# Performance work log

Hardware: AMD Instinct MI355X
Metric: run time of the kernel (lower is better)

The kernel has to match this reference:

```python
import jax, jax.numpy as jnp
import numpy as np

B, T, D, H = 4, 2048, 1024, 16
HS = D // H  # head_size = 64
EPS = 1e-5


def _layernorm(x, g, b):
    mu = jnp.mean(x, axis=-1, keepdims=True)
    var = jnp.var(x, axis=-1, keepdims=True)
    return (x - mu) * jax.lax.rsqrt(var + EPS) * g + b


def setup_inputs() -> dict:
    key = jax.random.key(0)
    ks = jax.random.split(key, 12)
    s = lambda fan_in: 1.0 / np.sqrt(fan_in)
    return {
        "x": jax.random.normal(ks[0], (B, T, D), dtype=jnp.float32),
        # per-head projections, stacked: (H, D, HS)
        "Wq": jax.random.uniform(ks[1], (H, D, HS), jnp.float32, -s(D), s(D)),
        "Wk": jax.random.uniform(ks[2], (H, D, HS), jnp.float32, -s(D), s(D)),
        "Wv": jax.random.uniform(ks[3], (H, D, HS), jnp.float32, -s(D), s(D)),
        "Wo": jax.random.uniform(ks[4], (D, D), jnp.float32, -s(D), s(D)),
        "bo": jax.random.uniform(ks[5], (D,), jnp.float32, -s(D), s(D)),
        "W1": jax.random.uniform(ks[6], (D, 4 * D), jnp.float32, -s(D), s(D)),
        "b1": jax.random.uniform(ks[7], (4 * D,), jnp.float32, -s(D), s(D)),
        "W2": jax.random.uniform(ks[8], (4 * D, D), jnp.float32, -s(4 * D), s(4 * D)),
        "b2": jax.random.uniform(ks[9], (D,), jnp.float32, -s(4 * D), s(4 * D)),
        "g1": jnp.ones((D,), jnp.float32),
        "be1": jnp.zeros((D,), jnp.float32),
        "g2": jnp.ones((D,), jnp.float32),
        "be2": jnp.zeros((D,), jnp.float32),
    }


def reference(x, Wq, Wk, Wv, Wo, bo, W1, b1, W2, b2, g1, be1, g2, be2):
    # --- self-attention sublayer (pre-LN) ---
    h = _layernorm(x, g1, be1)                       # (B,T,D)
    q = jnp.einsum('btd,hds->bhts', h, Wq)           # (B,H,T,HS)
    k = jnp.einsum('btd,hds->bhts', h, Wk)
    v = jnp.einsum('btd,hds->bhts', h, Wv)
    scores = jnp.einsum('bhts,bhus->bhtu', q, k) * (HS ** -0.5)  # (B,H,T,T)
    causal = jnp.tril(jnp.ones((T, T), dtype=bool))
    scores = jnp.where(causal, scores, -jnp.inf)
    w = jax.nn.softmax(scores, axis=-1)
    attn = jnp.einsum('bhtu,bhus->bhts', w, v)       # (B,H,T,HS)
    attn = attn.transpose(0, 2, 1, 3).reshape(B, T, D)  # concat heads
    x = x + attn @ Wo + bo
    # --- feed-forward sublayer (pre-LN) ---
    h2 = _layernorm(x, g2, be2)
    x = x + jax.nn.relu(h2 @ W1 + b1) @ W2 + b2
    return x
```

## Files before the change

### kernel.cpp

```cpp
#include <hip/hip_runtime.h>
#include <hip/hip_bf16.h>
#include <cstddef>

#define B_ 4
#define T_ 2048
#define D_ 1024
#define H_ 16
#define HS_ 64
#define QS_ 3072

typedef short short8 __attribute__((ext_vector_type(8)));
typedef float f32x4 __attribute__((ext_vector_type(4)));

__device__ __forceinline__ unsigned short f2b(float x) {
    __hip_bfloat16 b = __float2bfloat16(x);
    return *reinterpret_cast<unsigned short*>(&b);
}

__device__ __forceinline__ void gload_lds16(const void* g, void* l) {
    __builtin_amdgcn_global_load_lds((const __attribute__((address_space(1))) void*)g,
                                     (__attribute__((address_space(3))) void*)l, 16, 0, 0);
}

__global__ __launch_bounds__(256) void ln_kernel(const float* __restrict__ X,
                                                 const float* __restrict__ g,
                                                 const float* __restrict__ be,
                                                 unsigned short* __restrict__ O)
{
    const int row = blockIdx.x;
    const int tid = threadIdx.x;
    const float* xr = X + (size_t)row * D_;
    float4 xv = *reinterpret_cast<const float4*>(xr + tid * 4);
    float s  = xv.x + xv.y + xv.z + xv.w;
    float s2 = xv.x * xv.x + xv.y * xv.y + xv.z * xv.z + xv.w * xv.w;
#pragma unroll
    for (int off = 32; off > 0; off >>= 1) {
        s  += __shfl_xor(s,  off);
        s2 += __shfl_xor(s2, off);
    }
    __shared__ float red[8];
    const int wid = tid >> 6, lane = tid & 63;
    if (lane == 0) { red[wid * 2] = s; red[wid * 2 + 1] = s2; }
    __syncthreads();
    s  = red[0] + red[2] + red[4] + red[6];
    s2 = red[1] + red[3] + red[5] + red[7];
    const float mu  = s * (1.0f / D_);
    const float var = s2 * (1.0f / D_) - mu * mu;
    const float r   = rsqrtf(var + 1e-5f);
    float4 gv = *reinterpret_cast<const float4*>(g  + tid * 4);
    float4 bv = *reinterpret_cast<const float4*>(be + tid * 4);
    ushort4 ov;
    ov.x = f2b((xv.x - mu) * r * gv.x + bv.x);
    ov.y = f2b((xv.y - mu) * r * gv.y + bv.y);
    ov.z = f2b((xv.z - mu) * r * gv.z + bv.z);
    ov.w = f2b((xv.w - mu) * r * gv.w + bv.w);
    *reinterpret_cast<ushort4*>(O + (size_t)row * D_ + tid * 4) = ov;
}

__global__ __launch_bounds__(256) void transpose_all(const float* __restrict__ Wq,
                                                     const float* __restrict__ Wk,
                                                     const float* __restrict__ Wv,
                                                     const float* __restrict__ Wo,
                                                     const float* __restrict__ W1,
                                                     const float* __restrict__ W2,
                                                     unsigned short* __restrict__ Wtqkv,
                                                     unsigned short* __restrict__ Wto,
                                                     unsigned short* __restrict__ Wt1,
                                                     unsigned short* __restrict__ Wt2)
{
    __shared__ float tile[32][33];
    const int tx = threadIdx.x & 31, ty = threadIdx.x >> 5;
    int s = blockIdx.x;

    if (s < 3072) {
        const float* in = (s < 1024) ? Wq : (s < 2048) ? Wk : Wv;
        const int noff = (s < 1024) ? 0 : (s < 2048) ? D_ : 2 * D_;
        s &= 1023;
        const int bn = (s & 31) * 32, bk = (s >> 5) * 32;
        const int head = bn >> 6, s0 = bn & 63;
#pragma unroll
        for (int i = 0; i < 32; i += 8)
            tile[ty + i][tx] = in[(size_t)head * D_ * HS_ + (size_t)(bk + ty + i) * HS_ + s0 + tx];
        __syncthreads();
#pragma unroll
        for (int i = 0; i < 32; i += 8)
            Wtqkv[(size_t)(noff + bn + ty + i) * D_ + bk + tx] = f2b(tile[tx][ty + i]);
        return;
    }
    s -= 3072;
    const float* in; unsigned short* out; int K, N, bn, bk;
    if (s < 1024)      { in = Wo; out = Wto; K = D_;     N = D_;     bn = (s & 31) * 32;  bk = (s >> 5) * 32; }
    else if (s < 5120) { s -= 1024; in = W1; out = Wt1; K = D_;     N = 4 * D_; bn = (s & 127) * 32; bk = (s >> 7) * 32; }
    else               { s -= 5120; in = W2; out = Wt2; K = 4 * D_; N = D_;     bn = (s & 31) * 32;  bk = (s >> 5) * 32; }
#pragma unroll
    for (int i = 0; i < 32; i += 8)
        tile[ty + i][tx] = in[(size_t)(bk + ty + i) * N + bn + tx];
    __syncthreads();
#pragma unroll
    for (int i = 0; i < 32; i += 8)
        out[(size_t)(bn + ty + i) * K + bk + tx] = f2b(tile[tx][ty + i]);
}

template<bool BIAS, bool RELU, bool RESID, bool OUT_BF16, bool SCALEQ>
__global__ __launch_bounds__(512, 1) void gemm_sq(const unsigned short* __restrict__ A,
                                                  const unsigned short* __restrict__ Bt,
                                                  const float* __restrict__ bias,
                                                  const float* __restrict__ resid,
                                                  float* __restrict__ Cf,
                                                  unsigned short* __restrict__ Cb,
                                                  int M, int N, int K)
{
    constexpr int BUFS = 16384 + 16384;
    __shared__ __attribute__((aligned(128))) unsigned short lds[2 * BUFS];

    const int tid = threadIdx.x, l = tid & 63, w = tid >> 6;
    const int wRow = w >> 2, wCol = w & 3;
    const int lr = l & 15, lq = l >> 4;

    const int gx = gridDim.x;
    const int nwg = gx * (int)gridDim.y;
    const int orig = (int)blockIdx.y * gx + (int)blockIdx.x;
    const int xcd = orig & 7, lo = orig >> 3;
    const int q8 = nwg >> 3, r8 = nwg & 7;
    const int wg = (xcd < r8 ? xcd * (q8 + 1) : r8 * (q8 + 1) + (xcd - r8) * q8) + lo;
    const int bm = wg / gx, bn = wg % gx;

    const int nt = K >> 6;

    auto ISSUE_HALF = [&](int t, int half) {
        const size_t kof = (size_t)t * 64;
        const int buf = t & 1;
        const unsigned short* src = (half < 2) ? A : Bt;
        const int rb = ((half < 2) ? bm : bn) * 256 + (half & 1) * 128;
        const int lb = buf * BUFS + ((half >= 2) ? 16384 : 0) + (half & 1) * 128 * 64;
#pragma unroll
        for (int p = 0; p < 2; ++p) {
            const int j = p * 512 + tid;
            const int row = j >> 3, ci = j & 7;
            gload_lds16(src + (size_t)(rb + row) * K + kof + ((ci ^ (row & 7)) * 8),
                        &lds[lb + j * 8]);
        }
    };

    f32x4 acc[8][4];
#pragma unroll
    for (int i = 0; i < 8; ++i)
#pragma unroll
        for (int j = 0; j < 4; ++j) acc[i][j] = (f32x4){0.f, 0.f, 0.f, 0.f};

    short8 af[4][2], bf[4][2];
    const int swz = lr & 7;

#pragma unroll
    for (int h = 0; h < 4; ++h) ISSUE_HALF(0, h);

    for (int t = 0; t < nt; ++t) {
        const unsigned short* As = &lds[(t & 1) * BUFS];
        const unsigned short* Bs = As + 16384;
        const bool more = (t + 1 < nt);

        asm volatile("s_waitcnt vmcnt(0)" ::: "memory");
        __builtin_amdgcn_s_barrier();

        if (more) ISSUE_HALF(t + 1, 0);
#pragma unroll
        for (int mi = 0; mi < 4; ++mi) {
            const int row = wRow * 128 + mi * 16 + lr;
#pragma unroll
            for (int ks = 0; ks < 2; ++ks)
                af[mi][ks] = *reinterpret_cast<const short8*>(&As[row * 64 + (((ks * 4 + lq) ^ swz) * 8)]);
        }
#pragma unroll
        for (int nj = 0; nj < 2; ++nj) {
            const int rowB = wCol * 64 + nj * 16 + lr;
#pragma unroll
            for (int ks = 0; ks < 2; ++ks)
                bf[nj][ks] = *reinterpret_cast<const short8*>(&Bs[rowB * 64 + (((ks * 4 + lq) ^ swz) * 8)]);
        }
        asm volatile("s_waitcnt lgkmcnt(0)" ::: "memory");
        __builtin_amdgcn_sched_barrier(0);
        __builtin_amdgcn_s_setprio(1);
#pragma unroll
        for (int mi = 0; mi < 4; ++mi)
#pragma unroll
            for (int nj = 0; nj < 2; ++nj)
#pragma unroll
                for (int ks = 0; ks < 2; ++ks)
                    acc[mi][nj] = __builtin_amdgcn_mfma_f32_16x16x32_bf16(af[mi][ks], bf[nj][ks], acc[mi][nj], 0, 0, 0);
        __builtin_amdgcn_s_setprio(0);

        if (more) ISSUE_HALF(t + 1, 1);
#pragma unroll
        for (int nj = 2; nj < 4; ++nj) {
            const int rowB = wCol * 64 + nj * 16 + lr;
#pragma unroll
            for (int ks = 0; ks < 2; ++ks)
                bf[nj][ks] = *reinterpret_cast<const short8*>(&Bs[rowB * 64 + (((ks * 4 + lq) ^ swz) * 8)]);
        }
        asm volatile("s_waitcnt lgkmcnt(0)" ::: "memory");
        __builtin_amdgcn_sched_barrier(0);
        __builtin_amdgcn_s_setprio(1);
#pragma unroll
        for (int mi = 0; mi < 4; ++mi)
#pragma unroll
            for (int nj = 2; nj < 4; ++nj)
#pragma unroll
                for (int ks = 0; ks < 2; ++ks)
                    acc[mi][nj] = __builtin_amdgcn_mfma_f32_16x16x32_bf16(af[mi][ks], bf[nj][ks], acc[mi][nj], 0, 0, 0);
        __builtin_amdgcn_s_setprio(0);

        if (more) { ISSUE_HALF(t + 1, 2); ISSUE_HALF(t + 1, 3); }
#pragma unroll
        for (int mi = 0; mi < 4; ++mi) {
            const int row = wRow * 128 + (4 + mi) * 16 + lr;
#pragma unroll
            for (int ks = 0; ks < 2; ++ks)
                af[mi][ks] = *reinterpret_cast<const short8*>(&As[row * 64 + (((ks * 4 + lq) ^ swz) * 8)]);
        }
        asm volatile("s_waitcnt lgkmcnt(0)" ::: "memory");
        __builtin_amdgcn_sched_barrier(0);
        __builtin_amdgcn_s_setprio(1);
#pragma unroll
        for (int mi = 0; mi < 4; ++mi)
#pragma unroll
            for (int nj = 0; nj < 2; ++nj)
#pragma unroll
                for (int ks = 0; ks < 2; ++ks)
                    acc[4 + mi][nj] = __builtin_amdgcn_mfma_f32_16x16x32_bf16(af[mi][ks], bf[nj][ks], acc[4 + mi][nj], 0, 0, 0);
        __builtin_amdgcn_s_setprio(0);

        __builtin_amdgcn_s_setprio(1);
#pragma unroll
        for (int mi = 0; mi < 4; ++mi)
#pragma unroll
            for (int nj = 2; nj < 4; ++nj)
#pragma unroll
                for (int ks = 0; ks < 2; ++ks)
                    acc[4 + mi][nj] = __builtin_amdgcn_mfma_f32_16x16x32_bf16(af[mi][ks], bf[nj][ks], acc[4 + mi][nj], 0, 0, 0);
        __builtin_amdgcn_s_setprio(0);
    }

    const int m0 = bm * 256 + wRow * 128;
    const int n0 = bn * 256 + wCol * 64;
#pragma unroll
    for (int nf = 0; nf < 4; ++nf) {
        const int col = n0 + nf * 16 + lr;
        const float bv = BIAS ? bias[col] : 0.0f;
#pragma unroll
        for (int mf = 0; mf < 8; ++mf) {
#pragma unroll
            for (int r = 0; r < 4; ++r) {
                const int row = m0 + mf * 16 + lq * 4 + r;
                float c = acc[mf][nf][r] + bv;
                if (RELU) c = fmaxf(c, 0.0f);
                if (RESID) c += resid[(size_t)row * N + col];
                if (SCALEQ) { if (col < D_) c *= 0.18033688f; }
                if (OUT_BF16) Cb[(size_t)row * N + col] = f2b(c);
                else          Cf[(size_t)row * N + col] = c;
            }
        }
    }
}

template<bool BIAS, bool RELU, bool RESID, bool OUT_BF16, bool SCALEQ>
__global__ __launch_bounds__(512, 1) void gemm_sq2(const unsigned short* __restrict__ A,
                                                   const unsigned short* __restrict__ Bt,
                                                   const float* __restrict__ bias,
                                                   const float* __restrict__ resid,
                                                   float* __restrict__ Cf,
                                                   unsigned short* __restrict__ Cb,
                                                   int M, int N, int K)
{
    constexpr int BUFS = 8192 + 16384;
    __shared__ __attribute__((aligned(128))) unsigned short lds[3 * BUFS];

    const int tid = threadIdx.x, l = tid & 63, w = tid >> 6;
    const int wRow = w >> 2, wCol = w & 3;
    const int lr = l & 15, lq = l >> 4;

    const int gx = gridDim.x;
    const int nwg = gx * (int)gridDim.y;
    const int orig = (int)blockIdx.y * gx + (int)blockIdx.x;
    const int xcd = orig & 7, lo = orig >> 3;
    const int q8 = nwg >> 3, r8 = nwg & 7;
    const int wg = (xcd < r8 ? xcd * (q8 + 1) : r8 * (q8 + 1) + (xcd - r8) * q8) + lo;
    const int bm = wg / gx, bn = wg % gx;

    const int nt = K >> 6;

    auto ISSUE = [&](int t, int buf) {
        const size_t kof = (size_t)t * 64;
#pragma unroll
        for (int p = 0; p < 2; ++p) {
            const int j = p * 512 + tid;
            const int row = j >> 3, ci = j & 7;
            gload_lds16(A + (size_t)(bm * 128 + row) * K + kof + ((ci ^ (row & 7)) * 8),
                        &lds[buf * BUFS + j * 8]);
        }
#pragma unroll
        for (int p = 0; p < 4; ++p) {
            const int j = p * 512 + tid;
            const int row = j >> 3, ci = j & 7;
            gload_lds16(Bt + (size_t)(bn * 256 + row) * K + kof + ((ci ^ (row & 7)) * 8),
                        &lds[buf * BUFS + 8192 + j * 8]);
        }
    };

    f32x4 acc[4][4];
#pragma unroll
    for (int i = 0; i < 4; ++i)
#pragma unroll
        for (int j = 0; j < 4; ++j) acc[i][j] = (f32x4){0.f, 0.f, 0.f, 0.f};

    short8 af[2][2], bf[4][2];
    const int swz = lr & 7;

    ISSUE(0, 0);
    ISSUE(1, 1);

    for (int t = 0; t < nt; ++t) {
        const unsigned short* As = &lds[(t % 3) * BUFS];
        const unsigned short* Bs = As + 8192;
        if (t + 1 < nt) asm volatile("s_waitcnt vmcnt(6)" ::: "memory");
        else            asm volatile("s_waitcnt vmcnt(0)" ::: "memory");
        __builtin_amdgcn_s_barrier();
        if (t + 2 < nt) ISSUE(t + 2, (t + 2) % 3);

#pragma unroll
        for (int mi = 0; mi < 2; ++mi) {
            const int row = wRow * 64 + mi * 16 + lr;
#pragma unroll
            for (int ks = 0; ks < 2; ++ks)
                af[mi][ks] = *reinterpret_cast<const short8*>(&As[row * 64 + (((ks * 4 + lq) ^ swz) * 8)]);
        }
#pragma unroll
        for (int nj = 0; nj < 4; ++nj) {
            const int rowB = wCol * 64 + nj * 16 + lr;
#pragma unroll
            for (int ks = 0; ks < 2; ++ks)
                bf[nj][ks] = *reinterpret_cast<const short8*>(&Bs[rowB * 64 + (((ks * 4 + lq) ^ swz) * 8)]);
        }
        asm volatile("s_waitcnt lgkmcnt(0)" ::: "memory");
        __builtin_amdgcn_sched_barrier(0);
        __builtin_amdgcn_s_setprio(1);
#pragma unroll
        for (int mi = 0; mi < 2; ++mi)
#pragma unroll
            for (int nj = 0; nj < 4; ++nj)
#pragma unroll
                for (int ks = 0; ks < 2; ++ks)
                    acc[mi][nj] = __builtin_amdgcn_mfma_f32_16x16x32_bf16(af[mi][ks], bf[nj][ks], acc[mi][nj], 0, 0, 0);
        __builtin_amdgcn_s_setprio(0);

#pragma unroll
        for (int mi = 0; mi < 2; ++mi) {
            const int row = wRow * 64 + (2 + mi) * 16 + lr;
#pragma unroll
            for (int ks = 0; ks < 2; ++ks)
                af[mi][ks] = *reinterpret_cast<const short8*>(&As[row * 64 + (((ks * 4 + lq) ^ swz) * 8)]);
        }
        asm volatile("s_waitcnt lgkmcnt(0)" ::: "memory");
        __builtin_amdgcn_sched_barrier(0);
        __builtin_amdgcn_s_setprio(1);
#pragma unroll
        for (int mi = 0; mi < 2; ++mi)
#pragma unroll
            for (int nj = 0; nj < 4; ++nj)
#pragma unroll
                for (int ks = 0; ks < 2; ++ks)
                    acc[2 + mi][nj] = __builtin_amdgcn_mfma_f32_16x16x32_bf16(af[mi][ks], bf[nj][ks], acc[2 + mi][nj], 0, 0, 0);
        __builtin_amdgcn_s_setprio(0);
    }

    const int m0 = bm * 128 + wRow * 64;
    const int n0 = bn * 256 + wCol * 64;
#pragma unroll
    for (int nf = 0; nf < 4; ++nf) {
        const int col = n0 + nf * 16 + lr;
        const float bv = BIAS ? bias[col] : 0.0f;
#pragma unroll
        for (int mf = 0; mf < 4; ++mf) {
#pragma unroll
            for (int r = 0; r < 4; ++r) {
                const int row = m0 + mf * 16 + lq * 4 + r;
                float c = acc[mf][nf][r] + bv;
                if (RELU) c = fmaxf(c, 0.0f);
                if (RESID) c += resid[(size_t)row * N + col];
                if (SCALEQ) { if (col < D_) c *= 0.18033688f; }
                if (OUT_BF16) Cb[(size_t)row * N + col] = f2b(c);
                else          Cf[(size_t)row * N + col] = c;
            }
        }
    }
}

template<bool MASKED>
__device__ __forceinline__ void attn_chunk(
    const unsigned short* __restrict__ ksb,
    const unsigned short (* __restrict__ vsb)[72],
    unsigned short (* __restrict__ psw)[72],
    const short8* aq, f32x4* o,
    int lr, int lq, int wl)
{
    const short8 vone = {0x3F80, 0x3F80, 0x3F80, 0x3F80, 0x3F80, 0x3F80, 0x3F80, 0x3F80};
    f32x4 s[4];
#pragma unroll
    for (int kb = 0; kb < 4; ++kb) s[kb] = (f32x4){0.f, 0.f, 0.f, 0.f};
    __builtin_amdgcn_s_setprio(1);
#pragma unroll
    for (int kb = 0; kb < 4; ++kb) {
        if (MASKED && kb > wl) continue;
        const int row = kb * 16 + lr;
        const int sw = row & 7;
#pragma unroll
        for (int ks = 0; ks < 2; ++ks) {
            const int ch = (ks * 4 + lq) ^ sw;
            const short8 bk = *reinterpret_cast<const short8*>(&ksb[row * 64 + ch * 8]);
            s[kb] = __builtin_amdgcn_mfma_f32_16x16x32_bf16(aq[ks], bk, s[kb], 0, 0, 0);
        }
    }
    __builtin_amdgcn_s_setprio(0);

#pragma unroll
    for (int r = 0; r < 4; ++r) {
        const int qloc = wl * 16 + lq * 4 + r;
        float p[4];
#pragma unroll
        for (int kb = 0; kb < 4; ++kb) {
            const bool msk = MASKED && (kb * 16 + lr > qloc);
            p[kb] = msk ? 0.0f : exp2f(s[kb][r]);
        }
        const unsigned int w0 = (unsigned int)f2b(p[0]) | ((unsigned int)f2b(p[1]) << 16);
        const unsigned int w1 = (unsigned int)f2b(p[2]) | ((unsigned int)f2b(p[3]) << 16);
        uint2 pk; pk.x = w0; pk.y = w1;
        *reinterpret_cast<uint2*>(&psw[lq * 4 + r][lr * 4]) = pk;
    }
    asm volatile("s_waitcnt lgkmcnt(0)" ::: "memory");
    __builtin_amdgcn_s_setprio(1);
#pragma unroll
    for (int ks = 0; ks < 2; ++ks) {
        const short8 pa = *reinterpret_cast<const short8*>(&psw[lr][ks * 32 + lq * 8]);
#pragma unroll
        for (int df = 0; df < 4; ++df) {
            const short8 vb = *reinterpret_cast<const short8*>(&vsb[df * 16 + lr][ks * 32 + lq * 8]);
            o[df] = __builtin_amdgcn_mfma_f32_16x16x32_bf16(pa, vb, o[df], 0, 0, 0);
        }
        o[4] = __builtin_amdgcn_mfma_f32_16x16x32_bf16(pa, vone, o[4], 0, 0, 0);
    }
    __builtin_amdgcn_s_setprio(0);
}

__global__ __launch_bounds__(512, 4) void attn_mfma(const unsigned short* __restrict__ QKV,
                                                    unsigned short* __restrict__ Og)
{
    __shared__ __attribute__((aligned(128))) unsigned short Ks[2][64 * 64];
    __shared__ __attribute__((aligned(16)))  unsigned short Vs[2][64][72];
    __shared__ __attribute__((aligned(16)))  unsigned short Ps[8][16][72];

    const int NQT = T_ / 128;
    const int px = blockIdx.x;
    const int qtA = px, qtB = NQT - 1 - px;
    const int h = blockIdx.y, b = blockIdx.z;
    const int tid = threadIdx.x, w = tid >> 6, l = tid & 63;
    const int wl = w & 3, qsub = w >> 2;
    const int lr = l & 15, lq = l >> 4;
    const size_t base = (size_t)b * T_ * QS_ + h * HS_;

    short8 aqA[2], aqB[2];
    {
        const int qrl = qsub * 64 + wl * 16 + lr;
        const unsigned short* pA = QKV + base + (size_t)(qtA * 128 + qrl) * QS_;
        const unsigned short* pB = QKV + base + (size_t)(qtB * 128 + qrl) * QS_;
        aqA[0] = *reinterpret_cast<const short8*>(pA + lq * 8);
        aqA[1] = *reinterpret_cast<const short8*>(pA + 32 + lq * 8);
        aqB[0] = *reinterpret_cast<const short8*>(pB + lq * 8);
        aqB[1] = *reinterpret_cast<const short8*>(pB + 32 + lq * 8);
    }

    const unsigned short* Kg = QKV + D_;
    const unsigned short* Vg = QKV + 2 * D_;

    auto stage = [&](int c, int bf) {
        const int kbase = c * 64;
        {
            const int row = tid >> 3;
            const int c8 = ((tid & 7) ^ (row & 7)) * 8;
            gload_lds16(Kg + base + (size_t)(kbase + row) * QS_ + c8,
                        &Ks[bf][tid * 8]);
        }
        {
            const int vkey = tid & 63, vd0 = (tid >> 6) * 8;
            const int jkey = (vkey & 15) * 4 + (vkey >> 4);
            const unsigned short* vsrc = Vg + base + (size_t)(kbase + vkey) * QS_ + vd0;
            short8 v0 = *reinterpret_cast<const short8*>(vsrc);
#pragma unroll
            for (int jj = 0; jj < 8; ++jj) Vs[bf][vd0 + jj][jkey] = (unsigned short)v0[jj];
        }
    };

    stage(0, 0);
    __syncthreads();

    unsigned short (*psw)[72] = Ps[w];

    f32x4 oA[5], oB[5];
#pragma unroll
    for (int df = 0; df < 5; ++df) {
        oA[df] = (f32x4){0.f, 0.f, 0.f, 0.f};
        oB[df] = (f32x4){0.f, 0.f, 0.f, 0.f};
    }

    const int qminw = qsub * 64 + wl * 16;
    const int qmaxw = qminw + 15;

    const int nch = 2 * qtB + 2;
    int bf = 0;
    for (int c = 0; c < nch; ++c) {
        if (c + 1 < nch) stage(c + 1, bf ^ 1);
        const int relA = c * 64 - qtA * 128;
        const int relB = c * 64 - qtB * 128;
        if (relA <= qmaxw) {
            if (relA + 63 <= qminw)
                attn_chunk<false>(&Ks[bf][0], Vs[bf], psw, aqA, oA, lr, lq, wl);
            else
                attn_chunk<true>(&Ks[bf][0], Vs[bf], psw, aqA, oA, lr, lq, wl);
        }
        if (relB <= qmaxw) {
            if (relB + 63 <= qminw)
                attn_chunk<false>(&Ks[bf][0], Vs[bf], psw, aqB, oB, lr, lq, wl);
            else
                attn_chunk<true>(&Ks[bf][0], Vs[bf], psw, aqB, oB, lr, lq, wl);
        }
        if (c + 1 < nch) __syncthreads();
        bf ^= 1;
    }

    const size_t obase = (size_t)b * T_ * D_ + h * HS_;
#pragma unroll
    for (int r = 0; r < 4; ++r) {
        const float invA = 1.0f / oA[4][r];
        const float invB = 1.0f / oB[4][r];
        const int qrl = qsub * 64 + wl * 16 + lq * 4 + r;
        unsigned short* orowA = Og + obase + (size_t)(qtA * 128 + qrl) * D_;
        unsigned short* orowB = Og + obase + (size_t)(qtB * 128 + qrl) * D_;
#pragma unroll
        for (int df = 0; df < 4; ++df) {
            orowA[df * 16 + lr] = f2b(oA[df][r] * invA);
            orowB[df * 16 + lr] = f2b(oB[df][r] * invB);
        }
    }
}

extern "C" void kernel_launch(void* const* d_in, const int* in_sizes, int n_in,
                              void* d_out, int out_size, void* d_ws, size_t ws_size,
                              hipStream_t stream)
{
    const float* x   = (const float*)d_in[0];
    const float* Wq  = (const float*)d_in[1];
    const float* Wk  = (const float*)d_in[2];
    const float* Wv  = (const float*)d_in[3];
    const float* Wo  = (const float*)d_in[4];
    const float* bo  = (const float*)d_in[5];
    const float* W1  = (const float*)d_in[6];
    const float* b1  = (const float*)d_in[7];
    const float* W2  = (const float*)d_in[8];
    const float* b2  = (const float*)d_in[9];
    const float* g1  = (const float*)d_in[10];
    const float* be1 = (const float*)d_in[11];
    const float* g2  = (const float*)d_in[12];
    const float* be2 = (const float*)d_in[13];
    float* out = (float*)d_out;

    unsigned short* ws = (unsigned short*)d_ws;
    const size_t NT = (size_t)B_ * T_;
    unsigned short* hb    = ws;
    unsigned short* QKVb  = hb + NT * D_;
    unsigned short* Ab    = QKVb + NT * 3 * D_;
    unsigned short* f1    = QKVb;
    unsigned short* Wtqkv = Ab + NT * D_;
    unsigned short* Wto   = Wtqkv + (size_t)3 * D_ * D_;
    unsigned short* Wt1   = Wto + (size_t)D_ * D_;
    unsigned short* Wt2   = Wt1 + (size_t)4 * D_ * D_;

    dim3 b256(256), b512(512);

    transpose_all<<<dim3(12288), b256, 0, stream>>>(Wq, Wk, Wv, Wo, W1, W2,
                                                    Wtqkv, Wto, Wt1, Wt2);

    ln_kernel<<<NT, b256, 0, stream>>>(x, g1, be1, hb);

    gemm_sq2<false, false, false, true, true><<<dim3(3 * D_ / 256, NT / 128), b512, 0, stream>>>(
        hb, Wtqkv, nullptr, nullptr, nullptr, QKVb, (int)NT, 3 * D_, D_);

    attn_mfma<<<dim3(T_ / 256, H_, B_), b512, 0, stream>>>(QKVb, Ab);

    gemm_sq2<true, false, true, false, false><<<dim3(D_ / 256, NT / 128), b512, 0, stream>>>(
        Ab, Wto, bo, x, out, nullptr, (int)NT, D_, D_);

    ln_kernel<<<NT, b256, 0, stream>>>(out, g2, be2, hb);

    gemm_sq<true, true, false, true, false><<<dim3(4 * D_ / 256, NT / 256), b512, 0, stream>>>(
        hb, Wt1, b1, nullptr, nullptr, f1, (int)NT, 4 * D_, D_);

    gemm_sq2<true, false, true, false, false><<<dim3(D_ / 256, NT / 128), b512, 0, stream>>>(
        f1, Wt2, b2, out, out, nullptr, (int)NT, D_, 4 * D_);
}
```

Baseline: 342.7 us.

## Write V transposed from QKV GEMM epilogue and stage it via direct LDS loads

```diff
diff --git a/kernel.cpp b/kernel.cpp
--- a/kernel.cpp
+++ b/kernel.cpp
@@ -262,13 +262,14 @@
     }
 }
 
-template<bool BIAS, bool RELU, bool RESID, bool OUT_BF16, bool SCALEQ>
+template<bool BIAS, bool RELU, bool RESID, bool OUT_BF16, bool SCALEQ, bool VSPLIT>
 __global__ __launch_bounds__(512, 1) void gemm_sq2(const unsigned short* __restrict__ A,
                                                    const unsigned short* __restrict__ Bt,
                                                    const float* __restrict__ bias,
                                                    const float* __restrict__ resid,
                                                    float* __restrict__ Cf,
                                                    unsigned short* __restrict__ Cb,
+                                                   unsigned short* __restrict__ Vt,
                                                    int M, int N, int K)
 {
     constexpr int BUFS = 8192 + 16384;
@@ -387,8 +388,16 @@
                 if (RELU) c = fmaxf(c, 0.0f);
                 if (RESID) c += resid[(size_t)row * N + col];
                 if (SCALEQ) { if (col < D_) c *= 0.18033688f; }
-                if (OUT_BF16) Cb[(size_t)row * N + col] = f2b(c);
-                else          Cf[(size_t)row * N + col] = c;
+                if (VSPLIT && col >= 2 * D_) {
+                    const int hd = (col - 2 * D_) >> 6, sdim = (col - 2 * D_) & 63;
+                    const int bb = row >> 11, tt = row & (T_ - 1);
+                    const int sk = ((tt & 15) << 2) | ((tt >> 4) & 3);
+                    Vt[(((size_t)(bb * H_ + hd) * 64 + sdim) << 11) + (tt & ~63) + sk] = f2b(c);
+                } else if (OUT_BF16) {
+                    Cb[(size_t)row * N + col] = f2b(c);
+                } else {
+                    Cf[(size_t)row * N + col] = c;
+                }
             }
         }
     }
@@ -397,7 +406,7 @@
 template<bool MASKED>
 __device__ __forceinline__ void attn_chunk(
     const unsigned short* __restrict__ ksb,
-    const unsigned short (* __restrict__ vsb)[72],
+    const unsigned short* __restrict__ vsb,
     unsigned short (* __restrict__ psw)[72],
     const short8* aq, f32x4* o,
     int lr, int lq, int wl)
@@ -442,7 +451,9 @@
         const short8 pa = *reinterpret_cast<const short8*>(&psw[lr][ks * 32 + lq * 8]);
 #pragma unroll
         for (int df = 0; df < 4; ++df) {
-            const short8 vb = *reinterpret_cast<const short8*>(&vsb[df * 16 + lr][ks * 32 + lq * 8]);
+            const int vrow = df * 16 + lr;
+            const int vch = (ks * 4 + lq) ^ (vrow & 7);
+            const short8 vb = *reinterpret_cast<const short8*>(&vsb[vrow * 64 + vch * 8]);
             o[df] = __builtin_amdgcn_mfma_f32_16x16x32_bf16(pa, vb, o[df], 0, 0, 0);
         }
         o[4] = __builtin_amdgcn_mfma_f32_16x16x32_bf16(pa, vone, o[4], 0, 0, 0);
@@ -451,10 +462,11 @@
 }
 
 __global__ __launch_bounds__(512, 4) void attn_mfma(const unsigned short* __restrict__ QKV,
+                                                    const unsigned short* __restrict__ Vt,
                                                     unsigned short* __restrict__ Og)
 {
     __shared__ __attribute__((aligned(128))) unsigned short Ks[2][64 * 64];
-    __shared__ __attribute__((aligned(16)))  unsigned short Vs[2][64][72];
+    __shared__ __attribute__((aligned(128))) unsigned short Vs[2][64 * 64];
     __shared__ __attribute__((aligned(16)))  unsigned short Ps[8][16][72];
 
     const int NQT = T_ / 128;
@@ -478,24 +490,14 @@
     }
 
     const unsigned short* Kg = QKV + D_;
-    const unsigned short* Vg = QKV + 2 * D_;
+    const unsigned short* Vg = Vt + ((size_t)(b * H_ + h) * 64 << 11);
 
     auto stage = [&](int c, int bf) {
         const int kbase = c * 64;
-        {
-            const int row = tid >> 3;
-            const int c8 = ((tid & 7) ^ (row & 7)) * 8;
-            gload_lds16(Kg + base + (size_t)(kbase + row) * QS_ + c8,
-                        &Ks[bf][tid * 8]);
-        }
-        {
-            const int vkey = tid & 63, vd0 = (tid >> 6) * 8;
-            const int jkey = (vkey & 15) * 4 + (vkey >> 4);
-            const unsigned short* vsrc = Vg + base + (size_t)(kbase + vkey) * QS_ + vd0;
-            short8 v0 = *reinterpret_cast<const short8*>(vsrc);
-#pragma unroll
-            for (int jj = 0; jj < 8; ++jj) Vs[bf][vd0 + jj][jkey] = (unsigned short)v0[jj];
-        }
+        const int row = tid >> 3;
+        const int cx = ((tid & 7) ^ (row & 7)) * 8;
+        gload_lds16(Kg + base + (size_t)(kbase + row) * QS_ + cx, &Ks[bf][tid * 8]);
+        gload_lds16(Vg + ((size_t)row << 11) + kbase + cx, &Vs[bf][tid * 8]);
     };
 
     stage(0, 0);
@@ -521,15 +523,15 @@
         const int relB = c * 64 - qtB * 128;
         if (relA <= qmaxw) {
             if (relA + 63 <= qminw)
-                attn_chunk<false>(&Ks[bf][0], Vs[bf], psw, aqA, oA, lr, lq, wl);
+                attn_chunk<false>(&Ks[bf][0], &Vs[bf][0], psw, aqA, oA, lr, lq, wl);
             else
-                attn_chunk<true>(&Ks[bf][0], Vs[bf], psw, aqA, oA, lr, lq, wl);
+                attn_chunk<true>(&Ks[bf][0], &Vs[bf][0], psw, aqA, oA, lr, lq, wl);
         }
         if (relB <= qmaxw) {
             if (relB + 63 <= qminw)
-                attn_chunk<false>(&Ks[bf][0], Vs[bf], psw, aqB, oB, lr, lq, wl);
+                attn_chunk<false>(&Ks[bf][0], &Vs[bf][0], psw, aqB, oB, lr, lq, wl);
             else
-                attn_chunk<true>(&Ks[bf][0], Vs[bf], psw, aqB, oB, lr, lq, wl);
+                attn_chunk<true>(&Ks[bf][0], &Vs[bf][0], psw, aqB, oB, lr, lq, wl);
         }
         if (c + 1 < nch) __syncthreads();
         bf ^= 1;
@@ -581,6 +583,7 @@
     unsigned short* Wto   = Wtqkv + (size_t)3 * D_ * D_;
     unsigned short* Wt1   = Wto + (size_t)D_ * D_;
     unsigned short* Wt2   = Wt1 + (size_t)4 * D_ * D_;
+    unsigned short* Vtb   = Wt2 + (size_t)4 * D_ * D_;
 
     dim3 b256(256), b512(512);
 
@@ -589,19 +592,19 @@
 
     ln_kernel<<<NT, b256, 0, stream>>>(x, g1, be1, hb);
 
-    gemm_sq2<false, false, false, true, true><<<dim3(3 * D_ / 256, NT / 128), b512, 0, stream>>>(
-        hb, Wtqkv, nullptr, nullptr, nullptr, QKVb, (int)NT, 3 * D_, D_);
-
-    attn_mfma<<<dim3(T_ / 256, H_, B_), b512, 0, stream>>>(QKVb, Ab);
-
-    gemm_sq2<true, false, true, false, false><<<dim3(D_ / 256, NT / 128), b512, 0, stream>>>(
-        Ab, Wto, bo, x, out, nullptr, (int)NT, D_, D_);
+    gemm_sq2<false, false, false, true, true, true><<<dim3(3 * D_ / 256, NT / 128), b512, 0, stream>>>(
+        hb, Wtqkv, nullptr, nullptr, nullptr, QKVb, Vtb, (int)NT, 3 * D_, D_);
+
+    attn_mfma<<<dim3(T_ / 256, H_, B_), b512, 0, stream>>>(QKVb, Vtb, Ab);
+
+    gemm_sq2<true, false, true, false, false, false><<<dim3(D_ / 256, NT / 128), b512, 0, stream>>>(
+        Ab, Wto, bo, x, out, nullptr, nullptr, (int)NT, D_, D_);
 
     ln_kernel<<<NT, b256, 0, stream>>>(out, g2, be2, hb);
 
     gemm_sq<true, true, false, true, false><<<dim3(4 * D_ / 256, NT / 256), b512, 0, stream>>>(
         hb, Wt1, b1, nullptr, nullptr, f1, (int)NT, 4 * D_, D_);
 
-    gemm_sq2<true, false, true, false, false><<<dim3(D_ / 256, NT / 128), b512, 0, stream>>>(
-        f1, Wt2, b2, out, out, nullptr, (int)NT, D_, 4 * D_);
-}
+    gemm_sq2<true, false, true, false, false, false><<<dim3(D_ / 256, NT / 128), b512, 0, stream>>>(
+        f1, Wt2, b2, out, out, nullptr, nullptr, (int)NT, D_, 4 * D_);
+}
```

Measured after the change: 353.9 us. +3.3%, slower.
